# Optimization experiments

Measured on AMD Instinct MI355X. Metric: run time of the kernel, lower is better.

Reference implementation:

```python
import jax, jax.numpy as jnp
import numpy as np

B, N, E, H = 4, 1024, 1024, 16
D = E // H  # head dim = 64
SCALE = float(E) ** 0.5  # NOTE: original scales by embedding_dim**0.5, not head_dim


def setup_inputs() -> dict:
    key = jax.random.key(0)
    ks = jax.random.split(key, 9)
    sd = 1.0 / np.sqrt(E)
    return {
        "q": jax.random.normal(ks[0], (B, N, E), jnp.float32),
        "k": jax.random.normal(ks[1], (B, N, E), jnp.float32),
        "v": jax.random.normal(ks[2], (B, N, E), jnp.float32),
        "Wq": jax.random.normal(ks[3], (E, E), jnp.float32) * sd,
        "bq": jax.random.normal(ks[4], (E,), jnp.float32) * sd,
        "Wk": jax.random.normal(ks[5], (E, E), jnp.float32) * sd,
        "bk": jax.random.normal(ks[6], (E,), jnp.float32) * sd,
        "Wv": jax.random.normal(ks[7], (E, E), jnp.float32) * sd,
        "bv": jax.random.normal(ks[8], (E,), jnp.float32) * sd,
    }


def _split_heads(x):
    # (b, n, h*d) -> (b, h, n, d)
    b, n, _ = x.shape
    return x.reshape(b, n, H, D).transpose(0, 2, 1, 3)


def reference(q, k, v, Wq, bq, Wk, bk, Wv, bv):
    q = _split_heads(q @ Wq.T + bq)
    k = _split_heads(k @ Wk.T + bk)
    v = _split_heads(v @ Wv.T + bv)
    # full NxN scores, scaled by embedding_dim**0.5 (as in original)
    attn = jnp.einsum('bhnd,bhld->bhnl', q, k) / SCALE
    attn = jax.nn.softmax(attn, axis=-1)
    # dropout omitted (eval mode)
    # faithful to original non-standard einsum: sums attn over l, broadcasts v
    out = jnp.einsum('bhnl,bhnd->bhnd', attn, v)
    return (out, attn)
```

## Files before the change

### kernel.cpp

```cpp
#include <hip/hip_runtime.h>
#include <hip/hip_bf16.h>
#include <math.h>

#define Bc 4
#define Nc 1024
#define Ec 1024
#define Hc 16
#define Dc 64
#define Mc 4096
#define OUT0_ELEMS 4194304
#define ATTN_ELEMS 67108864ULL
#define SCRATCH_OFF 58720256
#define NTK 32

typedef __attribute__((ext_vector_type(4))) float f32x4;
typedef __attribute__((ext_vector_type(16))) float f32x16;
typedef __attribute__((ext_vector_type(8))) short s16x8;

__device__ __forceinline__ short f2bf(float f) {
    union { __bf16 h; short s; } c; c.h = (__bf16)f; return c.s;
}

typedef const __attribute__((address_space(1))) char gch;
typedef __attribute__((address_space(3))) char lch;
__device__ __forceinline__ void gload16(const short* g, short* l) {
    __builtin_amdgcn_global_load_lds((gch*)g, (lch*)l, 16, 0, 0);
}

__global__ __launch_bounds__(256)
void cvt_kernel(const float* __restrict__ xq, const float* __restrict__ xk,
                const float* __restrict__ wq, const float* __restrict__ wk,
                short* __restrict__ dst)
{
    const int which = blockIdx.y;
    const float* src; size_t n, off;
    switch (which) {
      case 0:  src = xq; n = 4194304; off = 0;       break;
      case 1:  src = xk; n = 4194304; off = 4194304; break;
      case 2:  src = wq; n = 1048576; off = 8388608; break;
      default: src = wk; n = 1048576; off = 9437184; break;
    }
    const size_t i = ((size_t)blockIdx.x * 256 + threadIdx.x) * 8;
    if (i >= n) return;
    f32x4 a = *(const f32x4*)(src + i);
    f32x4 b = *(const f32x4*)(src + i + 4);
    s16x8 o;
    o[0] = f2bf(a[0]); o[1] = f2bf(a[1]); o[2] = f2bf(a[2]); o[3] = f2bf(a[3]);
    o[4] = f2bf(b[0]); o[5] = f2bf(b[1]); o[6] = f2bf(b[2]); o[7] = f2bf(b[3]);
    *(s16x8*)(dst + off + i) = o;
}

__global__ __launch_bounds__(256)
void proj_kernel(const short* __restrict__ xall, const short* __restrict__ wall,
                 const float* __restrict__ bq, const float* __restrict__ bk,
                 short* __restrict__ qws, short* __restrict__ kws)
{
    const int sel = blockIdx.z;
    const short* X = xall + (size_t)sel * 4194304;
    const short* W = wall + (size_t)sel * 1048576;
    const float* bias = (sel == 0) ? bq : bk;

    __shared__ __align__(16) short lA[3][128 * 32];
    __shared__ __align__(16) short lB[3][128 * 32];

    const int t    = threadIdx.x;
    const int lane = t & 63;
    const int w    = t >> 6;
    const int wr   = w >> 1, wc = w & 1;
    const int li   = lane & 15, g = lane >> 4;
    const int bm   = blockIdx.x * 128;
    const int bn   = blockIdx.y * 128;

    const int sr = lane >> 2;
    const int c_ = lane & 3;

    f32x4 acc[4][4];
#pragma unroll
    for (int i = 0; i < 4; ++i)
#pragma unroll
        for (int j = 0; j < 4; ++j)
            acc[i][j] = (f32x4){0.f, 0.f, 0.f, 0.f};

#define STAGE(buf, kt)                                                        \
    {                                                                         \
        const int kb = (kt) * 32;                                             \
        _Pragma("unroll")                                                     \
        for (int j = 0; j < 2; ++j) {                                         \
            const int row = w * 32 + j * 16 + sr;                             \
            const int cg  = (c_ ^ ((row >> 1) & 3)) * 8;                      \
            gload16(X + (size_t)(bm + row) * Ec + kb + cg,                    \
                    &lA[buf][(w * 32 + j * 16) * 32]);                        \
            gload16(W + (size_t)(bn + row) * Ec + kb + cg,                    \
                    &lB[buf][(w * 32 + j * 16) * 32]);                        \
        }                                                                     \
    }

    STAGE(0, 0);
    STAGE(1, 1);
    asm volatile("s_waitcnt vmcnt(4)" ::: "memory");
    __builtin_amdgcn_s_barrier();

    for (int kt = 0; kt < NTK; ++kt) {
        const int cur = kt % 3;
        if (kt + 2 < NTK) STAGE((kt + 2) % 3, kt + 2);

        s16x8 aF[4], bF[4];
#pragma unroll
        for (int mt = 0; mt < 4; ++mt) {
            const int r = wr * 64 + mt * 16 + li;
            aF[mt] = *(const s16x8*)&lA[cur][r * 32 + ((g ^ ((r >> 1) & 3)) * 8)];
        }
#pragma unroll
        for (int nt = 0; nt < 4; ++nt) {
            const int r = wc * 64 + nt * 16 + li;
            bF[nt] = *(const s16x8*)&lB[cur][r * 32 + ((g ^ ((r >> 1) & 3)) * 8)];
        }
#pragma unroll
        for (int mt = 0; mt < 4; ++mt)
#pragma unroll
            for (int nt = 0; nt < 4; ++nt)
                acc[mt][nt] = __builtin_amdgcn_mfma_f32_16x16x32_bf16(
                    aF[mt], bF[nt], acc[mt][nt], 0, 0, 0);

        if (kt + 2 < NTK) {
            asm volatile("s_waitcnt vmcnt(4)" ::: "memory");
        } else {
            asm volatile("s_waitcnt vmcnt(0)" ::: "memory");
        }
        __builtin_amdgcn_s_barrier();
    }
#undef STAGE

    short* dstBF = (sel == 0) ? qws : kws;
#pragma unroll
    for (int nt = 0; nt < 4; ++nt) {
        const int col = bn + wc * 64 + nt * 16 + li;
        const float bcol = bias[col];
        const int h = col >> 6, d = col & 63;
#pragma unroll
        for (int mt = 0; mt < 4; ++mt) {
#pragma unroll
            for (int r = 0; r < 4; ++r) {
                const int row = bm + wr * 64 + mt * 16 + g * 4 + r;
                const int bb = row >> 10, n = row & 1023;
                const size_t off = ((size_t)(bb * Hc + h) * Nc + n) * Dc + d;
                dstBF[off] = f2bf(acc[mt][nt][r] + bcol);
            }
        }
    }
}

__global__ __launch_bounds__(512, 4)
void fused_kernel(const short* __restrict__ qws, const short* __restrict__ kws,
                  float* __restrict__ attnOut,
                  const float* __restrict__ vin, const float* __restrict__ Wv,
                  const float* __restrict__ bv, float* __restrict__ out0)
{
    __shared__ __align__(16) short lsA[2][128 * 32];
    __shared__ __align__(16) short lsB[2][128 * 32];
    __shared__ float red[8][32];

    const int bid = blockIdx.x;
    const int t   = threadIdx.x;
    const int lane = t & 63;

    if (bid < 256) {
        const int bm = (bid & 31) * 128;
        const int bn = (bid >> 5) * 128;
        const int w  = t >> 6;
        const int wr = w >> 2;
        const int wc = w & 3;
        const int li = lane & 15, g = lane >> 4;

        const int r0 = t >> 2;
        const int c2 = t & 3;
        const float* Xs = vin + (size_t)(bm + r0) * Ec + c2 * 8;
        const float* Ws = Wv  + (size_t)(bn + r0) * Ec + c2 * 8;
        const int aoff = r0 * 32 + ((c2 ^ ((r0 >> 1) & 3)) * 8);

        f32x4 acc[4][2];
#pragma unroll
        for (int i = 0; i < 4; ++i)
#pragma unroll
            for (int j = 0; j < 2; ++j)
                acc[i][j] = (f32x4){0.f, 0.f, 0.f, 0.f};

        f32x4 eA0, eA1, eB0, eB1;
        f32x4 oA0, oA1, oB0, oB1;

#define VLOAD(a0, a1, b0, b1, kt)                                             \
        {                                                                     \
            const float* pa = Xs + (kt) * 32;                                 \
            const float* pb = Ws + (kt) * 32;                                 \
            a0 = *(const f32x4*)(pa); a1 = *(const f32x4*)(pa + 4);           \
            b0 = *(const f32x4*)(pb); b1 = *(const f32x4*)(pb + 4);           \
        }

#define VWRITE(buf, a0, a1, b0, b1)                                           \
        {                                                                     \
            s16x8 ha, hb;                                                     \
            _Pragma("unroll")                                                 \
            for (int i = 0; i < 4; ++i) {                                     \
                ha[i] = f2bf(a0[i]); ha[i + 4] = f2bf(a1[i]);                 \
                hb[i] = f2bf(b0[i]); hb[i + 4] = f2bf(b1[i]);                 \
            }                                                                 \
            *(s16x8*)&lsA[buf][aoff] = ha;                                    \
            *(s16x8*)&lsB[buf][aoff] = hb;                                    \
        }

#define VCOMPUTE(buf)                                                         \
        {                                                                     \
            s16x8 aF[4], bF[2];                                               \
            _Pragma("unroll")                                                 \
            for (int mt = 0; mt < 4; ++mt) {                                  \
                const int r = wr * 64 + mt * 16 + li;                         \
                aF[mt] = *(const s16x8*)&lsA[buf][r * 32 + ((g ^ ((r >> 1) & 3)) * 8)]; \
            }                                                                 \
            _Pragma("unroll")                                                 \
            for (int nt = 0; nt < 2; ++nt) {                                  \
                const int r = wc * 32 + nt * 16 + li;                         \
                bF[nt] = *(const s16x8*)&lsB[buf][r * 32 + ((g ^ ((r >> 1) & 3)) * 8)]; \
            }                                                                 \
            _Pragma("unroll")                                                 \
            for (int mt = 0; mt < 4; ++mt)                                    \
                _Pragma("unroll")                                             \
                for (int nt = 0; nt < 2; ++nt)                                \
                    acc[mt][nt] = __builtin_amdgcn_mfma_f32_16x16x32_bf16(    \
                        aF[mt], bF[nt], acc[mt][nt], 0, 0, 0);                \
        }

        VLOAD(eA0, eA1, eB0, eB1, 0);
        VLOAD(oA0, oA1, oB0, oB1, 1);
        VWRITE(0, eA0, eA1, eB0, eB1);
        VLOAD(eA0, eA1, eB0, eB1, 2);
        asm volatile("s_waitcnt lgkmcnt(0)" ::: "memory");
        __builtin_amdgcn_s_barrier();

        for (int tt = 0; tt < NTK; tt += 2) {
            VCOMPUTE(0);
            if (tt + 1 < NTK) {
                VWRITE(1, oA0, oA1, oB0, oB1);
                if (tt + 3 < NTK) VLOAD(oA0, oA1, oB0, oB1, tt + 3);
            }
            asm volatile("s_waitcnt lgkmcnt(0)" ::: "memory");
            __builtin_amdgcn_s_barrier();

            if (tt + 1 < NTK) {
                VCOMPUTE(1);
                if (tt + 2 < NTK) {
                    VWRITE(0, eA0, eA1, eB0, eB1);
                    if (tt + 4 < NTK) VLOAD(eA0, eA1, eB0, eB1, tt + 4);
                }
                asm volatile("s_waitcnt lgkmcnt(0)" ::: "memory");
                __builtin_amdgcn_s_barrier();
            }
        }
#undef VCOMPUTE
#undef VWRITE
#undef VLOAD

#pragma unroll
        for (int nt = 0; nt < 2; ++nt) {
            const int col = bn + wc * 32 + nt * 16 + li;
            const float bcol = bv[col];
            const int h = col >> 6, d = col & 63;
#pragma unroll
            for (int mt = 0; mt < 4; ++mt) {
#pragma unroll
                for (int r = 0; r < 4; ++r) {
                    const int row = bm + wr * 64 + mt * 16 + g * 4 + r;
                    const int bb = row >> 10, n = row & 1023;
                    out0[((size_t)(bb * Hc + h) * Nc + n) * Dc + d] =
                        acc[mt][nt][r] + bcol;
                }
            }
        }
        return;
    }

    const int abid = bid - 256;
    const int rb  = (abid >> 3) & 31;
    const int bh  = ((abid & 7) << 3) | (abid >> 8);
    const int w  = t >> 6;
    const int li = lane & 31;
    const int hi = lane >> 5;

    const short* Qb = qws + (size_t)bh * (Nc * Dc);
    const short* Kb = kws + (size_t)bh * (Nc * Dc);

    s16x8 qF[4];
    {
        const short* qp = Qb + (size_t)(rb * 32 + li) * Dc + hi * 8;
#pragma unroll
        for (int s = 0; s < 4; ++s)
            qF[s] = *(const s16x8*)(qp + s * 16);
    }

    f32x16 acc[4];
#pragma unroll
    for (int i = 0; i < 4; ++i) acc[i] = (f32x16)(0.f);

    const int colbase = w * 128;
#pragma unroll
    for (int ct = 0; ct < 4; ++ct) {
        const short* kp = Kb + (size_t)(colbase + ct * 32 + li) * Dc + hi * 8;
#pragma unroll
        for (int s = 0; s < 4; ++s) {
            s16x8 kf = *(const s16x8*)(kp + s * 16);
            acc[ct] = __builtin_amdgcn_mfma_f32_32x32x16_bf16(qF[s], kf, acc[ct], 0, 0, 0);
        }
    }

    const float c = 1.44269504f / 32.0f;
    float sm[16];
#pragma unroll
    for (int r = 0; r < 16; ++r) sm[r] = 0.f;
#pragma unroll
    for (int ct = 0; ct < 4; ++ct) {
#pragma unroll
        for (int r = 0; r < 16; ++r) {
            float p = __builtin_amdgcn_exp2f(acc[ct][r] * c);
            acc[ct][r] = p;
            sm[r] += p;
        }
    }
#pragma unroll
    for (int r = 0; r < 16; ++r) {
#pragma unroll
        for (int off = 1; off < 32; off <<= 1)
            sm[r] += __shfl_xor(sm[r], off);
    }

    if (li == 0) {
#pragma unroll
        for (int r = 0; r < 16; ++r)
            red[w][(r & 3) + 8 * (r >> 2) + 4 * hi] = sm[r];
    }
    __syncthreads();
#pragma unroll
    for (int r = 0; r < 16; ++r) {
        const int row = (r & 3) + 8 * (r >> 2) + 4 * hi;
        float s = red[0][row] + red[1][row] + red[2][row] + red[3][row] +
                  red[4][row] + red[5][row] + red[6][row] + red[7][row];
        sm[r] = 1.0f / s;
    }

    float* outp = attnOut + (size_t)bh * (Nc * Nc) + (size_t)(rb * 32) * Nc;
#pragma unroll
    for (int ct = 0; ct < 4; ++ct) {
        const int col = colbase + ct * 32 + li;
#pragma unroll
        for (int r = 0; r < 16; ++r) {
            const int row = (r & 3) + 8 * (r >> 2) + 4 * hi;
            __builtin_nontemporal_store(acc[ct][r] * sm[r],
                                        &outp[(size_t)row * Nc + col]);
        }
    }
}

extern "C" void kernel_launch(void* const* d_in, const int* in_sizes, int n_in,
                              void* d_out, int out_size, void* d_ws, size_t ws_size,
                              hipStream_t stream) {
    const float* q  = (const float*)d_in[0];
    const float* k  = (const float*)d_in[1];
    const float* v  = (const float*)d_in[2];
    const float* Wq = (const float*)d_in[3];
    const float* bq = (const float*)d_in[4];
    const float* Wk = (const float*)d_in[5];
    const float* bk = (const float*)d_in[6];
    const float* Wv = (const float*)d_in[7];
    const float* bv = (const float*)d_in[8];

    float* out0 = (float*)d_out;
    float* attn = (float*)d_out + OUT0_ELEMS;

    short* s16  = (short*)(attn + SCRATCH_OFF);
    short* xall = s16;
    short* wall = s16 + 8388608;

    short* qws = (short*)d_ws;
    short* kws = qws + (size_t)Mc * Ec;

    cvt_kernel<<<dim3(2048, 4), 256, 0, stream>>>(q, k, Wq, Wk, s16);
    proj_kernel<<<dim3(32, 8, 2), 256, 0, stream>>>(
        xall, wall, bq, bk, qws, kws);
    fused_kernel<<<2304, 512, 0, stream>>>(qws, kws, attn, v, Wv, bv, out0);
}
```

Baseline: 118.8 us.

## Stage Q and K tiles through swizzled LDS in attention blocks

The attention-score path now loads Q and K into LDS with 16-byte global-to-LDS copies using an XOR swizzle, instead of each wave reading K fragments straight from global memory. K is staged in four 256-row tiles with barriers between them, and the column ownership per wave is remapped so each tile is spread across all waves. Shared memory is unified into one raw buffer aliased between the GEMM and attention branches. The goal is coalesced K/Q loads and less redundant global traffic, at the cost of extra barriers and serialized staging with no double buffering.

```diff
diff --git a/kernel.cpp b/kernel.cpp
--- a/kernel.cpp
+++ b/kernel.cpp
@@ -156,15 +156,16 @@
                   const float* __restrict__ vin, const float* __restrict__ Wv,
                   const float* __restrict__ bv, float* __restrict__ out0)
 {
-    __shared__ __align__(16) short lsA[2][128 * 32];
-    __shared__ __align__(16) short lsB[2][128 * 32];
-    __shared__ float red[8][32];
+    __shared__ __align__(16) char smemRaw[37888];
 
     const int bid = blockIdx.x;
     const int t   = threadIdx.x;
     const int lane = t & 63;
 
     if (bid < 256) {
+        short (*lsA)[128 * 32] = (short (*)[128 * 32])(smemRaw);
+        short (*lsB)[128 * 32] = (short (*)[128 * 32])(smemRaw + 16384);
+
         const int bm = (bid & 31) * 128;
         const int bn = (bid >> 5) * 128;
         const int w  = t >> 6;
@@ -278,6 +279,10 @@
         return;
     }
 
+    short* lsK = (short*)smemRaw;
+    short* lsQ = (short*)(smemRaw + 32768);
+    float (*red)[32] = (float (*)[32])(smemRaw + 36864);
+
     const int abid = bid - 256;
     const int rb  = (abid >> 3) & 31;
     const int bh  = ((abid & 7) << 3) | (abid >> 8);
@@ -288,28 +293,54 @@
     const short* Qb = qws + (size_t)bh * (Nc * Dc);
     const short* Kb = kws + (size_t)bh * (Nc * Dc);
 
+    const int gcs = ((lane & 7) ^ (lane >> 3)) * 8;
+    const int gr8 = lane >> 3;
+
+    if (w < 4)
+        gload16(Qb + (size_t)(rb * 32 + w * 8 + gr8) * Dc + gcs,
+                &lsQ[(w * 8) * Dc]);
+
+#define STAGEK(tile)                                                          \
+    {                                                                         \
+        _Pragma("unroll")                                                     \
+        for (int j = 0; j < 4; ++j) {                                         \
+            const int rb8 = w * 32 + j * 8;                                   \
+            gload16(Kb + (size_t)((tile) * 256 + rb8 + gr8) * Dc + gcs,       \
+                    &lsK[rb8 * Dc]);                                          \
+        }                                                                     \
+    }
+
+    STAGEK(0);
+    __syncthreads();
+
     s16x8 qF[4];
-    {
-        const short* qp = Qb + (size_t)(rb * 32 + li) * Dc + hi * 8;
-#pragma unroll
-        for (int s = 0; s < 4; ++s)
-            qF[s] = *(const s16x8*)(qp + s * 16);
+#pragma unroll
+    for (int s = 0; s < 4; ++s) {
+        const int slot = (hi + 2 * s) ^ (li & 7);
+        qF[s] = *(const s16x8*)&lsQ[li * Dc + slot * 8];
     }
 
     f32x16 acc[4];
 #pragma unroll
     for (int i = 0; i < 4; ++i) acc[i] = (f32x16)(0.f);
 
-    const int colbase = w * 128;
-#pragma unroll
-    for (int ct = 0; ct < 4; ++ct) {
-        const short* kp = Kb + (size_t)(colbase + ct * 32 + li) * Dc + hi * 8;
+#pragma unroll
+    for (int tile = 0; tile < 4; ++tile) {
+        const int lr = w * 32 + li;
 #pragma unroll
         for (int s = 0; s < 4; ++s) {
-            s16x8 kf = *(const s16x8*)(kp + s * 16);
-            acc[ct] = __builtin_amdgcn_mfma_f32_32x32x16_bf16(qF[s], kf, acc[ct], 0, 0, 0);
-        }
-    }
+            const int slot = (hi + 2 * s) ^ (li & 7);
+            s16x8 kf = *(const s16x8*)&lsK[lr * Dc + slot * 8];
+            acc[tile] = __builtin_amdgcn_mfma_f32_32x32x16_bf16(
+                qF[s], kf, acc[tile], 0, 0, 0);
+        }
+        __syncthreads();
+        if (tile < 3) {
+            STAGEK(tile + 1);
+            __syncthreads();
+        }
+    }
+#undef STAGEK
 
     const float c = 1.44269504f / 32.0f;
     float sm[16];
@@ -348,7 +379,7 @@
     float* outp = attnOut + (size_t)bh * (Nc * Nc) + (size_t)(rb * 32) * Nc;
 #pragma unroll
     for (int ct = 0; ct < 4; ++ct) {
-        const int col = colbase + ct * 32 + li;
+        const int col = ct * 256 + w * 32 + li;
 #pragma unroll
         for (int r = 0; r < 16; ++r) {
             const int row = (r & 3) + 8 * (r >> 2) + 4 * hi;
```

After: 115.5 us, median of 2. 2.8% less time.
